# Optimization experiments

Hardware: AMD Instinct MI355X
Metric: run time of the kernel (lower is better)

The kernel has to match this reference:

```python
import jax, jax.numpy as jnp
import numpy as np

B, T, I, H, C = 512, 256, 128, 64, 3  # batch, seq_len, input_size, hidden_size, num_classes


def _lstm_dir(x, w_ih, w_hh, b, reverse):
    """Single-direction LSTM over x: (B, T, D_in) -> (B, T, H).

    Gate order matches PyTorch: i, f, g, o. b = b_ih + b_hh (combined).
    Input-to-gate GEMM is hoisted out of the scan for efficiency.
    """
    xg = jnp.einsum('bti,gi->btg', x, w_ih) + b  # (B, T, 4H)
    if reverse:
        xg = xg[:, ::-1]
    xg_t = jnp.swapaxes(xg, 0, 1)  # (T, B, 4H)
    h0 = jnp.zeros((x.shape[0], w_hh.shape[1]), x.dtype)
    c0 = jnp.zeros_like(h0)

    def step(carry, g):
        h, c = carry
        g = g + h @ w_hh.T
        i, f, gg, o = jnp.split(g, 4, axis=-1)
        i = jax.nn.sigmoid(i)
        f = jax.nn.sigmoid(f)
        gg = jnp.tanh(gg)
        o = jax.nn.sigmoid(o)
        c = f * c + i * gg
        h = o * jnp.tanh(c)
        return (h, c), h

    _, hs = jax.lax.scan(step, (h0, c0), xg_t)  # (T, B, H)
    hs = jnp.swapaxes(hs, 0, 1)  # (B, T, H)
    if reverse:
        hs = hs[:, ::-1]
    return hs


def setup_inputs() -> dict:
    key = jax.random.key(0)
    ks = jax.random.split(key, 20)
    s = 1.0 / np.sqrt(H)  # PyTorch LSTM init scale
    d = {"x": jax.random.normal(ks[0], (B, T, I), dtype=jnp.float32)}
    i = 1
    for l, d_in in [(0, I), (1, 2 * H)]:
        for suf in ["f", "r"]:
            d[f"w_ih_l{l}{suf}"] = jax.random.uniform(ks[i], (4 * H, d_in), minval=-s, maxval=s); i += 1
            d[f"w_hh_l{l}{suf}"] = jax.random.uniform(ks[i], (4 * H, H), minval=-s, maxval=s); i += 1
            d[f"b_l{l}{suf}"] = jax.random.uniform(ks[i], (4 * H,), minval=-s, maxval=s); i += 1
    d["fc_w"] = jax.random.uniform(ks[i], (C, 2 * H), minval=-s, maxval=s); i += 1
    d["fc_b"] = jax.random.uniform(ks[i], (C,), minval=-s, maxval=s)
    return d


def reference(x, w_ih_l0f, w_hh_l0f, b_l0f, w_ih_l0r, w_hh_l0r, b_l0r,
              w_ih_l1f, w_hh_l1f, b_l1f, w_ih_l1r, w_hh_l1r, b_l1r,
              fc_w, fc_b):
    # Layer 0 (bidirectional)
    h0f = _lstm_dir(x, w_ih_l0f, w_hh_l0f, b_l0f, False)
    h0r = _lstm_dir(x, w_ih_l0r, w_hh_l0r, b_l0r, True)
    x1 = jnp.concatenate([h0f, h0r], axis=-1)  # (B, T, 2H)
    # (inter-layer dropout is identity in eval mode)
    # Layer 1 (bidirectional)
    h1f = _lstm_dir(x1, w_ih_l1f, w_hh_l1f, b_l1f, False)
    h1r = _lstm_dir(x1, w_ih_l1r, w_hh_l1r, b_l1r, True)
    out = jnp.concatenate([h1f, h1r], axis=-1)  # (B, T, 2H)
    last = out[:, -1, :]  # (B, 2H); dropout is identity in eval mode
    return last @ fc_w.T + fc_b  # (B, C) logits
```

## Files before the change

kernel.cpp:

```cpp
#include <hip/hip_runtime.h>

#define TT 256
#define BB 512
#define NG 256
#define KIN 128

typedef _Float16 half2v __attribute__((ext_vector_type(2)));
typedef _Float16 half4v __attribute__((ext_vector_type(4)));
typedef _Float16 half8v __attribute__((ext_vector_type(8)));
typedef float float4v __attribute__((ext_vector_type(4)));

__device__ __forceinline__ float sig_(float x){ return 1.f/(1.f+__expf(-x)); }
__device__ __forceinline__ float th_(float x){ return fmaf(2.f, 1.f/(1.f+__expf(-2.f*x)), -1.f); }

#if __has_builtin(__builtin_amdgcn_fdot2)
__device__ __forceinline__ float fdot2_(half2v a, half2v b, float c){
  return __builtin_amdgcn_fdot2(a, b, c, false);
}
#else
__device__ __forceinline__ float fdot2_(half2v a, half2v b, float c){
  return c + (float)a[0]*(float)b[0] + (float)a[1]*(float)b[1];
}
#endif

#define SV2(v,k) __builtin_shufflevector((v),(v), 2*(k), 2*(k)+1)

__device__ __forceinline__ half4v ld4h(const float* p){
  float4v v = *reinterpret_cast<const float4v*>(p);
  half4v h; h[0]=(_Float16)v[0]; h[1]=(_Float16)v[1]; h[2]=(_Float16)v[2]; h[3]=(_Float16)v[3];
  return h;
}

__global__ __launch_bounds__(256)
void conv_weights(const float* __restrict__ s0, const float* __restrict__ s1,
                  const float* __restrict__ s2, const float* __restrict__ s3,
                  const float* __restrict__ s4, const float* __restrict__ s5,
                  _Float16* __restrict__ dst)
{
  const int bid = blockIdx.x, tid = threadIdx.x;
  const float* src; int off, idx;
  if (bid < 128)      { src=s0; off=0;      idx=bid*256+tid; }
  else if (bid < 256) { src=s1; off=32768;  idx=(bid-128)*256+tid; }
  else if (bid < 384) { src=s2; off=65536;  idx=(bid-256)*256+tid; }
  else if (bid < 448) { src=s3; off=98304;  idx=(bid-384)*256+tid; }
  else if (bid < 512) { src=s4; off=114688; idx=(bid-448)*256+tid; }
  else                { src=s5; off=131072; idx=(bid-512)*256+tid; }
  dst[off+idx] = (_Float16)src[idx];
}

template<typename AT>
__global__ __launch_bounds__(256)
void gemm_xg(const AT* __restrict__ A, const _Float16* __restrict__ W16,
             const float* __restrict__ bias, _Float16* __restrict__ Cout)
{
  __shared__ __align__(16) _Float16 aL[64][72];
  __shared__ __align__(16) _Float16 wL[256][72];
  const int tid  = threadIdx.x;
  const int wave = tid >> 6;
  const int lane = tid & 63;
  const int lr   = lane & 15;
  const int kg   = lane >> 4;
  const size_t m0 = (size_t)blockIdx.x * 64;

  float4v acc[4][4];
  #pragma unroll
  for (int a=0;a<4;a++)
    #pragma unroll
    for (int b=0;b<4;b++)
      acc[a][b] = float4v{0.f,0.f,0.f,0.f};

  for (int kc = 0; kc < KIN; kc += 64) {
    if constexpr (__is_same(AT, float)) {
      #pragma unroll
      for (int q=0;q<4;q++){
        int fi = tid + q*256;
        int r = fi >> 4, c4 = (fi & 15)*4;
        *reinterpret_cast<half4v*>(&aL[r][c4]) = ld4h(&A[(m0+(size_t)r)*KIN + kc + c4]);
      }
    } else {
      #pragma unroll
      for (int q=0;q<2;q++){
        int fi = tid + q*256;
        int r = fi >> 3, c8 = (fi & 7)*8;
        *reinterpret_cast<half8v*>(&aL[r][c8]) =
            *reinterpret_cast<const half8v*>(&A[(m0+(size_t)r)*KIN + kc + c8]);
      }
    }
    #pragma unroll
    for (int q=0;q<8;q++){
      int fi = tid + q*256;
      int n = fi >> 3, c8 = (fi & 7)*8;
      *reinterpret_cast<half8v*>(&wL[n][c8]) =
          *reinterpret_cast<const half8v*>(&W16[(size_t)n*KIN + kc + c8]);
    }
    __syncthreads();
    #pragma unroll
    for (int ks=0; ks<64; ks+=32){
      half8v af[4], bf[4];
      #pragma unroll
      for (int rt=0;rt<4;rt++)
        af[rt] = *reinterpret_cast<const half8v*>(&aL[rt*16+lr][ks + kg*8]);
      #pragma unroll
      for (int ct=0;ct<4;ct++)
        bf[ct] = *reinterpret_cast<const half8v*>(&wL[wave*64 + ct*16 + lr][ks + kg*8]);
      #pragma unroll
      for (int rt=0;rt<4;rt++)
        #pragma unroll
        for (int ct=0;ct<4;ct++)
          acc[rt][ct] = __builtin_amdgcn_mfma_f32_16x16x32_f16(af[rt], bf[ct], acc[rt][ct], 0,0,0);
    }
    __syncthreads();
  }
  #pragma unroll
  for (int ct=0;ct<4;ct++){
    const int col = wave*64 + ct*16 + lr;
    const float bv = bias[col];
    #pragma unroll
    for (int rt=0;rt<4;rt++){
      const size_t rbase = m0 + rt*16 + kg*4;
      #pragma unroll
      for (int i=0;i<4;i++)
        Cout[(rbase+(size_t)i)*NG + col] = (_Float16)(acc[rt][ct][i] + bv);
    }
  }
}

template<int MODE>
__global__ __launch_bounds__(256, 4)
void lstm_scan_g4(const _Float16* __restrict__ xgPool,
                  const _Float16* __restrict__ whhPool,
                  int nF,
                  _Float16* __restrict__ x1out, float* __restrict__ hfin)
{
  const int tid = threadIdx.x;
  const int w   = tid >> 6;
  const int j   = tid & 63;
  const bool rev = (int)blockIdx.x >= nF;
  const int b = rev ? ((int)blockIdx.x - nF) : (int)blockIdx.x;
  const _Float16* xg  = xgPool  + (rev ? (size_t)BB*TT*NG : 0);
  const _Float16* whh = whhPool + (rev ? (size_t)16384 : 0);

  __shared__ __align__(16) float acts[2][256];
  __shared__ __align__(16) _Float16 hs4[4][64];

  half8v wreg[8];
  #pragma unroll
  for (int q=0;q<8;q++)
    wreg[q] = *reinterpret_cast<const half8v*>(&whh[(size_t)(w*64 + j)*64 + q*8]);

  hs4[w][j] = (_Float16)0.f;
  float c = 0.f, h_last = 0.f;

  const _Float16* xgb = xg + (size_t)b*TT*NG + w*64 + j;
  _Float16 ring[8];
  #pragma unroll
  for (int u=0;u<8;u++)
    ring[u] = xgb[(size_t)(rev ? (TT-1-u) : u) * NG];

  for (int tb=0; tb<TT; tb+=8){
    #pragma unroll
    for (int u=0;u<8;u++){
      const int tt = tb + u;
      const int t  = rev ? (TT-1-tt) : tt;

      const float xp = (float)ring[u];
      const int tf = tt + 8;
      if (tf < TT)
        ring[u] = xgb[(size_t)(rev ? (TT-1-tf) : tf) * NG];

      float a=0.f, a2=0.f;
      #pragma unroll
      for (int q=0;q<8;q++){
        const half8v h8 = *reinterpret_cast<const half8v*>(&hs4[w][q*8]);
        a  = fdot2_(SV2(wreg[q],0), SV2(h8,0), a);
        a2 = fdot2_(SV2(wreg[q],1), SV2(h8,1), a2);
        a  = fdot2_(SV2(wreg[q],2), SV2(h8,2), a);
        a2 = fdot2_(SV2(wreg[q],3), SV2(h8,3), a2);
      }
      const float pre = xp + (a + a2);
      acts[tt&1][w*64 + j] = (w==2) ? th_(pre) : sig_(pre);
      __syncthreads();

      const float iv = acts[tt&1][j];
      const float fv = acts[tt&1][64+j];
      const float gv = acts[tt&1][128+j];
      const float ov = acts[tt&1][192+j];
      c = fv*c + iv*gv;
      const float h = ov * th_(c);
      h_last = h;
      hs4[w][j] = (_Float16)h;
      if constexpr (MODE==0)
        if (w == 0)
          x1out[((size_t)b*TT + t)*128 + (rev ? 64 : 0) + j] = (_Float16)h;
    }
  }
  if constexpr (MODE==1)
    if (w == 0)
      hfin[(size_t)b*64 + j] = h_last;
}

__global__ __launch_bounds__(256)
void final_fuse(const _Float16* __restrict__ x1, const float* __restrict__ w_ih,
                const float* __restrict__ bvec, const float* __restrict__ hfin,
                const float* __restrict__ fcw, const float* __restrict__ fcb,
                float* __restrict__ out)
{
  const int b = blockIdx.x, tid = threadIdx.x;
  __shared__ float xs[128];
  __shared__ float act[256];
  __shared__ float hall[128];
  if (tid < 128) xs[tid] = (float)x1[((size_t)b*TT + (TT-1))*128 + tid];
  __syncthreads();
  float a = bvec[tid];
  #pragma unroll
  for (int kk=0;kk<32;kk++){
    float4v wv = *reinterpret_cast<const float4v*>(&w_ih[(size_t)tid*128 + kk*4]);
    a += wv[0]*xs[kk*4] + wv[1]*xs[kk*4+1] + wv[2]*xs[kk*4+2] + wv[3]*xs[kk*4+3];
  }
  const int grp = tid>>6;
  act[tid] = (grp==2) ? th_(a) : sig_(a);
  __syncthreads();
  if (tid < 64) {
    float c = act[tid]*act[128+tid];
    float h = act[192+tid]*th_(c);
    hall[64+tid] = h;
    hall[tid] = hfin[(size_t)b*64 + tid];
  }
  __syncthreads();
  if (tid < 3) {
    float acc2 = fcb[tid];
    for (int k=0;k<128;k++) acc2 += fcw[(size_t)tid*128 + k]*hall[k];
    out[(size_t)b*3 + tid] = acc2;
  }
}

extern "C" void kernel_launch(void* const* d_in, const int* in_sizes, int n_in,
                              void* d_out, int out_size, void* d_ws, size_t ws_size,
                              hipStream_t stream) {
  const float* x        = (const float*)d_in[0];
  const float* w_ih_l0f = (const float*)d_in[1];
  const float* w_hh_l0f = (const float*)d_in[2];
  const float* b_l0f    = (const float*)d_in[3];
  const float* w_ih_l0r = (const float*)d_in[4];
  const float* w_hh_l0r = (const float*)d_in[5];
  const float* b_l0r    = (const float*)d_in[6];
  const float* w_ih_l1f = (const float*)d_in[7];
  const float* w_hh_l1f = (const float*)d_in[8];
  const float* b_l1f    = (const float*)d_in[9];
  const float* w_ih_l1r = (const float*)d_in[10];
  const float* b_l1r    = (const float*)d_in[12];
  const float* fc_w     = (const float*)d_in[13];
  const float* fc_b     = (const float*)d_in[14];
  float* out = (float*)d_out;

  const size_t XG_BYTES = (size_t)BB*TT*NG*2;
  const size_t X1_BYTES = (size_t)BB*TT*128*2;
  const size_t HF_BYTES = (size_t)BB*64*4;
  const size_t W16_BYTES = (size_t)147456*2;
  if (ws_size < 2*XG_BYTES + X1_BYTES + HF_BYTES + W16_BYTES) return;
  _Float16* xgF  = (_Float16*)d_ws;
  _Float16* xgR  = (_Float16*)((char*)d_ws + XG_BYTES);
  _Float16* x1   = (_Float16*)((char*)d_ws + 2*XG_BYTES);
  float*    hfin = (float*)   ((char*)d_ws + 2*XG_BYTES + X1_BYTES);
  _Float16* w16  = (_Float16*)((char*)d_ws + 2*XG_BYTES + X1_BYTES + HF_BYTES);
  _Float16* wih_l0f16 = w16;
  _Float16* wih_l0r16 = w16 + 32768;
  _Float16* wih_l1f16 = w16 + 65536;
  _Float16* whh_l0f16 = w16 + 98304;
  _Float16* whh_l1f16 = w16 + 131072;

  const int MBLK = (BB*TT)/64;

  conv_weights<<<576, 256, 0, stream>>>(w_ih_l0f, w_ih_l0r, w_ih_l1f,
                                        w_hh_l0f, w_hh_l0r, w_hh_l1f, w16);
  gemm_xg<float><<<MBLK, 256, 0, stream>>>(x, wih_l0f16, b_l0f, xgF);
  gemm_xg<float><<<MBLK, 256, 0, stream>>>(x, wih_l0r16, b_l0r, xgR);
  lstm_scan_g4<0><<<1024, 256, 0, stream>>>(xgF, whh_l0f16, 512, x1, nullptr);
  gemm_xg<_Float16><<<MBLK, 256, 0, stream>>>(x1, wih_l1f16, b_l1f, xgF);
  lstm_scan_g4<1><<<512, 256, 0, stream>>>(xgF, whh_l1f16, 512, nullptr, hfin);
  final_fuse<<<BB, 256, 0, stream>>>(x1, w_ih_l1r, b_l1r, hfin, fc_w, fc_b, out);
}
```

Before: 402.8 us.

## Batch 16 sequences per block in LSTM scan using MFMA recurrent matmul

Replaces the per-sequence fdot2 recurrence with a block handling 16 batch rows, computing h·W_hh via MFMA 16x16x32 f16 with weights held in registers and h in swizzled LDS. Gate activations are exchanged through LDS in fp16 with two barriers per step. This cuts redundant weight traffic and instruction count per sequence, but launches far fewer blocks (64/32), leaving most CUs idle during the latency-bound serial scan, and stores activations in half precision.

Result: slower. 747.2 us (+85.5%).

```diff
diff --git a/kernel.cpp b/kernel.cpp
--- a/kernel.cpp
+++ b/kernel.cpp
@@ -12,18 +12,6 @@
 
 __device__ __forceinline__ float sig_(float x){ return 1.f/(1.f+__expf(-x)); }
 __device__ __forceinline__ float th_(float x){ return fmaf(2.f, 1.f/(1.f+__expf(-2.f*x)), -1.f); }
-
-#if __has_builtin(__builtin_amdgcn_fdot2)
-__device__ __forceinline__ float fdot2_(half2v a, half2v b, float c){
-  return __builtin_amdgcn_fdot2(a, b, c, false);
-}
-#else
-__device__ __forceinline__ float fdot2_(half2v a, half2v b, float c){
-  return c + (float)a[0]*(float)b[0] + (float)a[1]*(float)b[1];
-}
-#endif
-
-#define SV2(v,k) __builtin_shufflevector((v),(v), 2*(k), 2*(k)+1)
 
 __device__ __forceinline__ half4v ld4h(const float* p){
   float4v v = *reinterpret_cast<const float4v*>(p);
@@ -126,77 +114,131 @@
 }
 
 template<int MODE>
-__global__ __launch_bounds__(256, 4)
-void lstm_scan_g4(const _Float16* __restrict__ xgPool,
+__global__ __launch_bounds__(512, 1)
+void lstm_scan_mf(const _Float16* __restrict__ xgPool,
                   const _Float16* __restrict__ whhPool,
                   int nF,
                   _Float16* __restrict__ x1out, float* __restrict__ hfin)
 {
   const int tid = threadIdx.x;
   const int w   = tid >> 6;
-  const int j   = tid & 63;
+  const int l   = tid & 63;
+  const int g   = w >> 1;
+  const int nh  = w & 1;
+  const int lr  = l & 15;
+  const int kg  = l >> 4;
   const bool rev = (int)blockIdx.x >= nF;
-  const int b = rev ? ((int)blockIdx.x - nF) : (int)blockIdx.x;
+  const int bblk = rev ? ((int)blockIdx.x - nF) : (int)blockIdx.x;
+  const int b0 = bblk * 16;
   const _Float16* xg  = xgPool  + (rev ? (size_t)BB*TT*NG : 0);
   const _Float16* whh = whhPool + (rev ? (size_t)16384 : 0);
 
-  __shared__ __align__(16) float acts[2][256];
-  __shared__ __align__(16) _Float16 hs4[4][64];
-
-  half8v wreg[8];
-  #pragma unroll
-  for (int q=0;q<8;q++)
-    wreg[q] = *reinterpret_cast<const half8v*>(&whh[(size_t)(w*64 + j)*64 + q*8]);
-
-  hs4[w][j] = (_Float16)0.f;
-  float c = 0.f, h_last = 0.f;
-
-  const _Float16* xgb = xg + (size_t)b*TT*NG + w*64 + j;
-  _Float16 ring[8];
-  #pragma unroll
-  for (int u=0;u<8;u++)
-    ring[u] = xgb[(size_t)(rev ? (TT-1-u) : u) * NG];
-
-  for (int tb=0; tb<TT; tb+=8){
-    #pragma unroll
-    for (int u=0;u<8;u++){
-      const int tt = tb + u;
-      const int t  = rev ? (TT-1-tt) : tt;
-
-      const float xp = (float)ring[u];
-      const int tf = tt + 8;
-      if (tf < TT)
-        ring[u] = xgb[(size_t)(rev ? (TT-1-tf) : tf) * NG];
-
-      float a=0.f, a2=0.f;
-      #pragma unroll
-      for (int q=0;q<8;q++){
-        const half8v h8 = *reinterpret_cast<const half8v*>(&hs4[w][q*8]);
-        a  = fdot2_(SV2(wreg[q],0), SV2(h8,0), a);
-        a2 = fdot2_(SV2(wreg[q],1), SV2(h8,1), a2);
-        a  = fdot2_(SV2(wreg[q],2), SV2(h8,2), a);
-        a2 = fdot2_(SV2(wreg[q],3), SV2(h8,3), a2);
-      }
-      const float pre = xp + (a + a2);
-      acts[tt&1][w*64 + j] = (w==2) ? th_(pre) : sig_(pre);
-      __syncthreads();
-
-      const float iv = acts[tt&1][j];
-      const float fv = acts[tt&1][64+j];
-      const float gv = acts[tt&1][128+j];
-      const float ov = acts[tt&1][192+j];
-      c = fv*c + iv*gv;
-      const float h = ov * th_(c);
-      h_last = h;
-      hs4[w][j] = (_Float16)h;
-      if constexpr (MODE==0)
-        if (w == 0)
-          x1out[((size_t)b*TT + t)*128 + (rev ? 64 : 0) + j] = (_Float16)h;
-    }
-  }
-  if constexpr (MODE==1)
-    if (w == 0)
-      hfin[(size_t)b*64 + j] = h_last;
+  __shared__ __align__(16) _Float16 h_lds[16*64];
+  __shared__ __align__(16) _Float16 acts[4*64*20];
+
+  const size_t colA = (size_t)g*64 + (size_t)nh*32 + (size_t)lr;
+  half8v bf00 = *reinterpret_cast<const half8v*>(&whh[(colA   )*64 +  0 + kg*8]);
+  half8v bf01 = *reinterpret_cast<const half8v*>(&whh[(colA   )*64 + 32 + kg*8]);
+  half8v bf10 = *reinterpret_cast<const half8v*>(&whh[(colA+16)*64 +  0 + kg*8]);
+  half8v bf11 = *reinterpret_cast<const half8v*>(&whh[(colA+16)*64 + 32 + kg*8]);
+  asm volatile("" : "+v"(bf00), "+v"(bf01), "+v"(bf10), "+v"(bf11));
+
+  char* hb = (char*)h_lds;
+  const int aswz  = (lr & 7) << 4;
+  const int aoff0 = (lr*128 +  0 + kg*16) ^ aswz;
+  const int aoff1 = (lr*128 + 64 + kg*16) ^ aswz;
+
+  const int awr0 = (g*64 + nh*32 +  0 + lr)*20 + kg*4;
+  const int awr1 = (g*64 + nh*32 + 16 + lr)*20 + kg*4;
+  const int ard0 = (  0 + l)*20 + 2*w;
+  const int ard1 = ( 64 + l)*20 + 2*w;
+  const int ard2 = (128 + l)*20 + 2*w;
+  const int ard3 = (192 + l)*20 + 2*w;
+  const int r0 = 2*w, r1 = 2*w+1;
+  const int hw0 = (r0*128 + l*2) ^ ((r0&7)<<4);
+  const int hw1 = (r1*128 + l*2) ^ ((r1&7)<<4);
+
+  const int t0 = rev ? (TT-1) : 0;
+  const ptrdiff_t dstep = rev ? -(ptrdiff_t)NG : (ptrdiff_t)NG;
+  const _Float16* p0 = xg + ((size_t)(b0 + kg*4 + 0)*TT + t0)*NG + colA;
+  const _Float16* p1 = xg + ((size_t)(b0 + kg*4 + 1)*TT + t0)*NG + colA;
+  const _Float16* p2 = xg + ((size_t)(b0 + kg*4 + 2)*TT + t0)*NG + colA;
+  const _Float16* p3 = xg + ((size_t)(b0 + kg*4 + 3)*TT + t0)*NG + colA;
+
+  half8v sA, sB;
+  sA[0]=p0[0];  sA[1]=p1[0];  sA[2]=p2[0];  sA[3]=p3[0];
+  sA[4]=p0[16]; sA[5]=p1[16]; sA[6]=p2[16]; sA[7]=p3[16];
+  p0+=dstep; p1+=dstep; p2+=dstep; p3+=dstep;
+  sB[0]=p0[0];  sB[1]=p1[0];  sB[2]=p2[0];  sB[3]=p3[0];
+  sB[4]=p0[16]; sB[5]=p1[16]; sB[6]=p2[16]; sB[7]=p3[16];
+  p0+=dstep; p1+=dstep; p2+=dstep; p3+=dstep;
+
+  ((unsigned*)h_lds)[tid] = 0u;
+  float c0 = 0.f, c1 = 0.f, hl0 = 0.f, hl1 = 0.f;
+  __syncthreads();
+
+#define SCAN_STEP(tt_, S_) do {                                              \
+    const int tt = (tt_);                                                    \
+    const int t  = rev ? (TT-1-tt) : tt;                                     \
+    half8v a0 = *reinterpret_cast<const half8v*>(hb + aoff0);                \
+    half8v a1 = *reinterpret_cast<const half8v*>(hb + aoff1);                \
+    float4v ac0, ac1;                                                        \
+    ac0[0]=(float)S_[0]; ac0[1]=(float)S_[1];                                \
+    ac0[2]=(float)S_[2]; ac0[3]=(float)S_[3];                                \
+    ac1[0]=(float)S_[4]; ac1[1]=(float)S_[5];                                \
+    ac1[2]=(float)S_[6]; ac1[3]=(float)S_[7];                                \
+    if (tt+2 < TT){                                                          \
+      S_[0]=p0[0];  S_[1]=p1[0];  S_[2]=p2[0];  S_[3]=p3[0];                 \
+      S_[4]=p0[16]; S_[5]=p1[16]; S_[6]=p2[16]; S_[7]=p3[16];                \
+      p0+=dstep; p1+=dstep; p2+=dstep; p3+=dstep;                            \
+    }                                                                        \
+    ac0 = __builtin_amdgcn_mfma_f32_16x16x32_f16(a0, bf00, ac0, 0,0,0);      \
+    ac0 = __builtin_amdgcn_mfma_f32_16x16x32_f16(a1, bf01, ac0, 0,0,0);      \
+    ac1 = __builtin_amdgcn_mfma_f32_16x16x32_f16(a0, bf10, ac1, 0,0,0);      \
+    ac1 = __builtin_amdgcn_mfma_f32_16x16x32_f16(a1, bf11, ac1, 0,0,0);      \
+    half4v pk0, pk1;                                                         \
+    if (g == 2){                                                             \
+      pk0[0]=(_Float16)th_(ac0[0]); pk0[1]=(_Float16)th_(ac0[1]);            \
+      pk0[2]=(_Float16)th_(ac0[2]); pk0[3]=(_Float16)th_(ac0[3]);            \
+      pk1[0]=(_Float16)th_(ac1[0]); pk1[1]=(_Float16)th_(ac1[1]);            \
+      pk1[2]=(_Float16)th_(ac1[2]); pk1[3]=(_Float16)th_(ac1[3]);            \
+    } else {                                                                 \
+      pk0[0]=(_Float16)sig_(ac0[0]); pk0[1]=(_Float16)sig_(ac0[1]);          \
+      pk0[2]=(_Float16)sig_(ac0[2]); pk0[3]=(_Float16)sig_(ac0[3]);          \
+      pk1[0]=(_Float16)sig_(ac1[0]); pk1[1]=(_Float16)sig_(ac1[1]);          \
+      pk1[2]=(_Float16)sig_(ac1[2]); pk1[3]=(_Float16)sig_(ac1[3]);          \
+    }                                                                        \
+    *reinterpret_cast<half4v*>(&acts[awr0]) = pk0;                           \
+    *reinterpret_cast<half4v*>(&acts[awr1]) = pk1;                           \
+    __syncthreads();                                                         \
+    const half2v vi = *reinterpret_cast<const half2v*>(&acts[ard0]);         \
+    const half2v vf = *reinterpret_cast<const half2v*>(&acts[ard1]);         \
+    const half2v vg = *reinterpret_cast<const half2v*>(&acts[ard2]);         \
+    const half2v vo = *reinterpret_cast<const half2v*>(&acts[ard3]);         \
+    c0 = (float)vf[0]*c0 + (float)vi[0]*(float)vg[0];                        \
+    c1 = (float)vf[1]*c1 + (float)vi[1]*(float)vg[1];                        \
+    const float h0 = (float)vo[0]*th_(c0);                                   \
+    const float h1 = (float)vo[1]*th_(c1);                                   \
+    *reinterpret_cast<_Float16*>(hb + hw0) = (_Float16)h0;                   \
+    *reinterpret_cast<_Float16*>(hb + hw1) = (_Float16)h1;                   \
+    if constexpr (MODE==0){                                                  \
+      const int xoff = rev ? 64 : 0;                                         \
+      x1out[((size_t)(b0+r0)*TT + t)*128 + xoff + l] = (_Float16)h0;         \
+      x1out[((size_t)(b0+r1)*TT + t)*128 + xoff + l] = (_Float16)h1;         \
+    } else { hl0 = h0; hl1 = h1; }                                           \
+    __syncthreads();                                                         \
+  } while(0)
+
+  for (int tb=0; tb<TT; tb+=2){
+    SCAN_STEP(tb,   sA);
+    SCAN_STEP(tb+1, sB);
+  }
+#undef SCAN_STEP
+
+  if constexpr (MODE==1){
+    hfin[(size_t)(b0+r0)*64 + l] = hl0;
+    hfin[(size_t)(b0+r1)*64 + l] = hl1;
+  }
 }
 
 __global__ __launch_bounds__(256)
@@ -275,8 +317,8 @@
                                         w_hh_l0f, w_hh_l0r, w_hh_l1f, w16);
   gemm_xg<float><<<MBLK, 256, 0, stream>>>(x, wih_l0f16, b_l0f, xgF);
   gemm_xg<float><<<MBLK, 256, 0, stream>>>(x, wih_l0r16, b_l0r, xgR);
-  lstm_scan_g4<0><<<1024, 256, 0, stream>>>(xgF, whh_l0f16, 512, x1, nullptr);
+  lstm_scan_mf<0><<<64, 512, 0, stream>>>(xgF, whh_l0f16, 32, x1, nullptr);
   gemm_xg<_Float16><<<MBLK, 256, 0, stream>>>(x1, wih_l1f16, b_l1f, xgF);
-  lstm_scan_g4<1><<<512, 256, 0, stream>>>(xgF, whh_l1f16, 512, nullptr, hfin);
+  lstm_scan_mf<1><<<32, 512, 0, stream>>>(xgF, whh_l1f16, 32, nullptr, hfin);
   final_fuse<<<BB, 256, 0, stream>>>(x1, w_ih_l1r, b_l1r, hfin, fc_w, fc_b, out);
 }
```

## Batch four sequences per LSTM scan block with LDS-resident transposed weights

Applied to the files above, without the earlier changes.

The recurrent scan now processes four batch rows per block. W_hh is stored transposed and interleaved in LDS and shared across those rows, and each thread computes one gate column for all four rows with packed fp16 FMA instead of fp32-accumulated fdot2. This cuts the block count fourfold and amortises weight and h reads across batch rows. In exchange it adds a second barrier per step, lowers occupancy (launch bounds 1, only 256/128 blocks for 256 CUs), and accumulates in fp16, which risks precision loss.

Measured after the change: 697.3 us. 1.73x slower.

```diff
diff --git a/kernel.cpp b/kernel.cpp
--- a/kernel.cpp
+++ b/kernel.cpp
@@ -13,17 +13,17 @@
 __device__ __forceinline__ float sig_(float x){ return 1.f/(1.f+__expf(-x)); }
 __device__ __forceinline__ float th_(float x){ return fmaf(2.f, 1.f/(1.f+__expf(-2.f*x)), -1.f); }
 
-#if __has_builtin(__builtin_amdgcn_fdot2)
-__device__ __forceinline__ float fdot2_(half2v a, half2v b, float c){
-  return __builtin_amdgcn_fdot2(a, b, c, false);
+#define SV2(v,k) __builtin_shufflevector((v),(v), 2*(k), 2*(k)+1)
+
+#if __has_builtin(__builtin_elementwise_fma)
+__device__ __forceinline__ half2v pkfma_(half2v a, half2v b, half2v c){
+  return __builtin_elementwise_fma(a, b, c);
 }
 #else
-__device__ __forceinline__ float fdot2_(half2v a, half2v b, float c){
-  return c + (float)a[0]*(float)b[0] + (float)a[1]*(float)b[1];
+__device__ __forceinline__ half2v pkfma_(half2v a, half2v b, half2v c){
+  return a*b + c;
 }
 #endif
-
-#define SV2(v,k) __builtin_shufflevector((v),(v), 2*(k), 2*(k)+1)
 
 __device__ __forceinline__ half4v ld4h(const float* p){
   float4v v = *reinterpret_cast<const float4v*>(p);
@@ -38,14 +38,20 @@
                   _Float16* __restrict__ dst)
 {
   const int bid = blockIdx.x, tid = threadIdx.x;
-  const float* src; int off, idx;
+  const float* src; int off, idx; bool tr = false;
   if (bid < 128)      { src=s0; off=0;      idx=bid*256+tid; }
   else if (bid < 256) { src=s1; off=32768;  idx=(bid-128)*256+tid; }
   else if (bid < 384) { src=s2; off=65536;  idx=(bid-256)*256+tid; }
-  else if (bid < 448) { src=s3; off=98304;  idx=(bid-384)*256+tid; }
-  else if (bid < 512) { src=s4; off=114688; idx=(bid-448)*256+tid; }
-  else                { src=s5; off=131072; idx=(bid-512)*256+tid; }
-  dst[off+idx] = (_Float16)src[idx];
+  else if (bid < 448) { src=s3; off=98304;  idx=(bid-384)*256+tid; tr=true; }
+  else if (bid < 512) { src=s4; off=114688; idx=(bid-448)*256+tid; tr=true; }
+  else                { src=s5; off=131072; idx=(bid-512)*256+tid; tr=true; }
+  if (!tr){
+    dst[off+idx] = (_Float16)src[idx];
+  } else {
+    const int col = idx >> 6, k = idx & 63;
+    const int kk = k >> 3, e = k & 7;
+    dst[off + (kk*256 + col)*8 + e] = (_Float16)src[idx];
+  }
 }
 
 template<typename AT>
@@ -126,77 +132,114 @@
 }
 
 template<int MODE>
-__global__ __launch_bounds__(256, 4)
-void lstm_scan_g4(const _Float16* __restrict__ xgPool,
-                  const _Float16* __restrict__ whhPool,
-                  int nF,
-                  _Float16* __restrict__ x1out, float* __restrict__ hfin)
+__global__ __launch_bounds__(256, 1)
+void lstm_scan_lds(const _Float16* __restrict__ xgPool,
+                   const _Float16* __restrict__ whhTP,
+                   int nF,
+                   _Float16* __restrict__ x1out, float* __restrict__ hfin)
 {
-  const int tid = threadIdx.x;
-  const int w   = tid >> 6;
-  const int j   = tid & 63;
+  const int l = threadIdx.x;
+  const int w = l >> 6;
+  const int j = l & 63;
   const bool rev = (int)blockIdx.x >= nF;
-  const int b = rev ? ((int)blockIdx.x - nF) : (int)blockIdx.x;
-  const _Float16* xg  = xgPool  + (rev ? (size_t)BB*TT*NG : 0);
-  const _Float16* whh = whhPool + (rev ? (size_t)16384 : 0);
-
-  __shared__ __align__(16) float acts[2][256];
-  __shared__ __align__(16) _Float16 hs4[4][64];
-
-  half8v wreg[8];
+  const int bblk = rev ? ((int)blockIdx.x - nF) : (int)blockIdx.x;
+  const int b0 = bblk * 4;
+  const _Float16* xg   = xgPool + (rev ? (size_t)BB*TT*NG : 0);
+  const _Float16* whhT = whhTP  + (rev ? (size_t)16384 : 0);
+
+  __shared__ __align__(16) _Float16 wlds[16384];
+  __shared__ __align__(16) float    acts[4][256];
+  __shared__ __align__(16) _Float16 hlds[4][64];
+
   #pragma unroll
-  for (int q=0;q<8;q++)
-    wreg[q] = *reinterpret_cast<const half8v*>(&whh[(size_t)(w*64 + j)*64 + q*8]);
-
-  hs4[w][j] = (_Float16)0.f;
+  for (int q=0;q<8;q++){
+    const int u = q*256 + l;
+    *reinterpret_cast<half8v*>(&wlds[u*8]) =
+        *reinterpret_cast<const half8v*>(&whhT[(size_t)u*8]);
+  }
+  if (l < 128) ((unsigned*)hlds)[l] = 0u;
   float c = 0.f, h_last = 0.f;
-
-  const _Float16* xgb = xg + (size_t)b*TT*NG + w*64 + j;
-  _Float16 ring[8];
-  #pragma unroll
-  for (int u=0;u<8;u++)
-    ring[u] = xgb[(size_t)(rev ? (TT-1-u) : u) * NG];
-
-  for (int tb=0; tb<TT; tb+=8){
-    #pragma unroll
-    for (int u=0;u<8;u++){
-      const int tt = tb + u;
-      const int t  = rev ? (TT-1-tt) : tt;
-
-      const float xp = (float)ring[u];
-      const int tf = tt + 8;
-      if (tf < TT)
-        ring[u] = xgb[(size_t)(rev ? (TT-1-tf) : tf) * NG];
-
-      float a=0.f, a2=0.f;
-      #pragma unroll
-      for (int q=0;q<8;q++){
-        const half8v h8 = *reinterpret_cast<const half8v*>(&hs4[w][q*8]);
-        a  = fdot2_(SV2(wreg[q],0), SV2(h8,0), a);
-        a2 = fdot2_(SV2(wreg[q],1), SV2(h8,1), a2);
-        a  = fdot2_(SV2(wreg[q],2), SV2(h8,2), a);
-        a2 = fdot2_(SV2(wreg[q],3), SV2(h8,3), a2);
-      }
-      const float pre = xp + (a + a2);
-      acts[tt&1][w*64 + j] = (w==2) ? th_(pre) : sig_(pre);
-      __syncthreads();
-
-      const float iv = acts[tt&1][j];
-      const float fv = acts[tt&1][64+j];
-      const float gv = acts[tt&1][128+j];
-      const float ov = acts[tt&1][192+j];
-      c = fv*c + iv*gv;
-      const float h = ov * th_(c);
-      h_last = h;
-      hs4[w][j] = (_Float16)h;
-      if constexpr (MODE==0)
-        if (w == 0)
-          x1out[((size_t)b*TT + t)*128 + (rev ? 64 : 0) + j] = (_Float16)h;
-    }
-  }
+  __syncthreads();
+
+  const int t0 = rev ? (TT-1) : 0;
+  const ptrdiff_t dstep = rev ? -(ptrdiff_t)NG : (ptrdiff_t)NG;
+  const _Float16* p0 = xg + ((size_t)(b0+0)*TT + t0)*NG + l;
+  const _Float16* p1 = xg + ((size_t)(b0+1)*TT + t0)*NG + l;
+  const _Float16* p2 = xg + ((size_t)(b0+2)*TT + t0)*NG + l;
+  const _Float16* p3 = xg + ((size_t)(b0+3)*TT + t0)*NG + l;
+
+  half4v sA, sB;
+  sA[0]=*p0; sA[1]=*p1; sA[2]=*p2; sA[3]=*p3;
+  p0+=dstep; p1+=dstep; p2+=dstep; p3+=dstep;
+  sB[0]=*p0; sB[1]=*p1; sB[2]=*p2; sB[3]=*p3;
+  p0+=dstep; p1+=dstep; p2+=dstep; p3+=dstep;
+
+#define SCAN_STEP(tt_, S_) do {                                               \
+    const int tt = (tt_);                                                     \
+    const int t  = rev ? (TT-1-tt) : tt;                                      \
+    const float xr0=(float)S_[0], xr1=(float)S_[1];                           \
+    const float xr2=(float)S_[2], xr3=(float)S_[3];                           \
+    if (tt+2 < TT){                                                           \
+      S_[0]=*p0; S_[1]=*p1; S_[2]=*p2; S_[3]=*p3;                             \
+      p0+=dstep; p1+=dstep; p2+=dstep; p3+=dstep;                             \
+    }                                                                         \
+    half2v a00={0,0},a01={0,0},a02={0,0},a03={0,0};                           \
+    half2v a10={0,0},a11={0,0},a12={0,0},a13={0,0};                           \
+    half2v a20={0,0},a21={0,0},a22={0,0},a23={0,0};                           \
+    half2v a30={0,0},a31={0,0},a32={0,0},a33={0,0};                           \
+    _Pragma("unroll")                                                         \
+    for (int kk=0;kk<8;kk++){                                                 \
+      const half8v w8 = *reinterpret_cast<const half8v*>(&wlds[(kk*256+l)*8]);\
+      const half8v h0 = *reinterpret_cast<const half8v*>(&hlds[0][kk*8]);     \
+      const half8v h1 = *reinterpret_cast<const half8v*>(&hlds[1][kk*8]);     \
+      const half8v h2 = *reinterpret_cast<const half8v*>(&hlds[2][kk*8]);     \
+      const half8v h3 = *reinterpret_cast<const half8v*>(&hlds[3][kk*8]);     \
+      a00=pkfma_(SV2(w8,0),SV2(h0,0),a00); a01=pkfma_(SV2(w8,1),SV2(h0,1),a01);\
+      a02=pkfma_(SV2(w8,2),SV2(h0,2),a02); a03=pkfma_(SV2(w8,3),SV2(h0,3),a03);\
+      a10=pkfma_(SV2(w8,0),SV2(h1,0),a10); a11=pkfma_(SV2(w8,1),SV2(h1,1),a11);\
+      a12=pkfma_(SV2(w8,2),SV2(h1,2),a12); a13=pkfma_(SV2(w8,3),SV2(h1,3),a13);\
+      a20=pkfma_(SV2(w8,0),SV2(h2,0),a20); a21=pkfma_(SV2(w8,1),SV2(h2,1),a21);\
+      a22=pkfma_(SV2(w8,2),SV2(h2,2),a22); a23=pkfma_(SV2(w8,3),SV2(h2,3),a23);\
+      a30=pkfma_(SV2(w8,0),SV2(h3,0),a30); a31=pkfma_(SV2(w8,1),SV2(h3,1),a31);\
+      a32=pkfma_(SV2(w8,2),SV2(h3,2),a32); a33=pkfma_(SV2(w8,3),SV2(h3,3),a33);\
+    }                                                                         \
+    const half2v s0 = (a00+a01)+(a02+a03);                                    \
+    const half2v s1 = (a10+a11)+(a12+a13);                                    \
+    const half2v s2 = (a20+a21)+(a22+a23);                                    \
+    const half2v s3 = (a30+a31)+(a32+a33);                                    \
+    const float pre0 = xr0 + (float)s0[0] + (float)s0[1];                     \
+    const float pre1 = xr1 + (float)s1[0] + (float)s1[1];                     \
+    const float pre2 = xr2 + (float)s2[0] + (float)s2[1];                     \
+    const float pre3 = xr3 + (float)s3[0] + (float)s3[1];                     \
+    if (w == 2){                                                              \
+      acts[0][l]=th_(pre0); acts[1][l]=th_(pre1);                             \
+      acts[2][l]=th_(pre2); acts[3][l]=th_(pre3);                             \
+    } else {                                                                  \
+      acts[0][l]=sig_(pre0); acts[1][l]=sig_(pre1);                           \
+      acts[2][l]=sig_(pre2); acts[3][l]=sig_(pre3);                           \
+    }                                                                         \
+    __syncthreads();                                                          \
+    const float iv = acts[w][j];                                              \
+    const float fv = acts[w][64+j];                                           \
+    const float gv = acts[w][128+j];                                          \
+    const float ov = acts[w][192+j];                                          \
+    c = fv*c + iv*gv;                                                         \
+    const float h = ov * th_(c);                                              \
+    h_last = h;                                                               \
+    hlds[w][j] = (_Float16)h;                                                 \
+    if constexpr (MODE==0)                                                    \
+      x1out[((size_t)(b0+w)*TT + t)*128 + (rev ? 64 : 0) + j] = (_Float16)h;  \
+    __syncthreads();                                                          \
+  } while(0)
+
+  for (int tb=0; tb<TT; tb+=2){
+    SCAN_STEP(tb,   sA);
+    SCAN_STEP(tb+1, sB);
+  }
+#undef SCAN_STEP
+
   if constexpr (MODE==1)
-    if (w == 0)
-      hfin[(size_t)b*64 + j] = h_last;
+    hfin[(size_t)(b0+w)*64 + j] = h_last;
 }
 
 __global__ __launch_bounds__(256)
@@ -266,8 +309,8 @@
   _Float16* wih_l0f16 = w16;
   _Float16* wih_l0r16 = w16 + 32768;
   _Float16* wih_l1f16 = w16 + 65536;
-  _Float16* whh_l0f16 = w16 + 98304;
-  _Float16* whh_l1f16 = w16 + 131072;
+  _Float16* whhT_l0f  = w16 + 98304;
+  _Float16* whhT_l1f  = w16 + 131072;
 
   const int MBLK = (BB*TT)/64;
 
@@ -275,8 +318,8 @@
                                         w_hh_l0f, w_hh_l0r, w_hh_l1f, w16);
   gemm_xg<float><<<MBLK, 256, 0, stream>>>(x, wih_l0f16, b_l0f, xgF);
   gemm_xg<float><<<MBLK, 256, 0, stream>>>(x, wih_l0r16, b_l0r, xgR);
-  lstm_scan_g4<0><<<1024, 256, 0, stream>>>(xgF, whh_l0f16, 512, x1, nullptr);
+  lstm_scan_lds<0><<<256, 256, 0, stream>>>(xgF, whhT_l0f, 128, x1, nullptr);
   gemm_xg<_Float16><<<MBLK, 256, 0, stream>>>(x1, wih_l1f16, b_l1f, xgF);
-  lstm_scan_g4<1><<<512, 256, 0, stream>>>(xgF, whh_l1f16, 512, nullptr, hfin);
+  lstm_scan_lds<1><<<128, 256, 0, stream>>>(xgF, whhT_l1f, 128, nullptr, hfin);
   final_fuse<<<BB, 256, 0, stream>>>(x1, w_ih_l1r, b_l1r, hfin, fc_w, fc_b, out);
 }
```

## Batch 16 sequences per block and use MFMA for recurrent LSTM matmul

Applied to the files above, without the earlier changes.

Replaces the per-sequence scan kernel, which used fdot2 with one batch row per block, with a kernel that handles 16 batch rows per block. The recurrent h@W_hh product runs on 16x16x32 f16 MFMA instructions, with W_hh staged in swizzled LDS and h double-buffered in LDS. Each lane now owns four gate columns across four batch rows, which removes the acts exchange and one barrier per step. The cost is a much smaller grid (64 and 32 blocks instead of 1024 and 512), so far fewer CUs are busy, and each serial step carries MFMA latency plus LDS reads of the full weight matrix.

Result: slower. 624.4 us (+55.0%).

```diff
diff --git a/kernel.cpp b/kernel.cpp
--- a/kernel.cpp
+++ b/kernel.cpp
@@ -12,18 +12,6 @@
 
 __device__ __forceinline__ float sig_(float x){ return 1.f/(1.f+__expf(-x)); }
 __device__ __forceinline__ float th_(float x){ return fmaf(2.f, 1.f/(1.f+__expf(-2.f*x)), -1.f); }
-
-#if __has_builtin(__builtin_amdgcn_fdot2)
-__device__ __forceinline__ float fdot2_(half2v a, half2v b, float c){
-  return __builtin_amdgcn_fdot2(a, b, c, false);
-}
-#else
-__device__ __forceinline__ float fdot2_(half2v a, half2v b, float c){
-  return c + (float)a[0]*(float)b[0] + (float)a[1]*(float)b[1];
-}
-#endif
-
-#define SV2(v,k) __builtin_shufflevector((v),(v), 2*(k), 2*(k)+1)
 
 __device__ __forceinline__ half4v ld4h(const float* p){
   float4v v = *reinterpret_cast<const float4v*>(p);
@@ -126,77 +114,159 @@
 }
 
 template<int MODE>
-__global__ __launch_bounds__(256, 4)
-void lstm_scan_g4(const _Float16* __restrict__ xgPool,
+__global__ __launch_bounds__(256, 1)
+void lstm_scan_mm(const _Float16* __restrict__ xgPool,
                   const _Float16* __restrict__ whhPool,
                   int nF,
                   _Float16* __restrict__ x1out, float* __restrict__ hfin)
 {
   const int tid = threadIdx.x;
   const int w   = tid >> 6;
-  const int j   = tid & 63;
+  const int l   = tid & 63;
+  const int lr  = l & 15;
+  const int kg  = l >> 4;
   const bool rev = (int)blockIdx.x >= nF;
-  const int b = rev ? ((int)blockIdx.x - nF) : (int)blockIdx.x;
+  const int bblk = rev ? ((int)blockIdx.x - nF) : (int)blockIdx.x;
+  const int b0 = bblk * 16;
   const _Float16* xg  = xgPool  + (rev ? (size_t)BB*TT*NG : 0);
   const _Float16* whh = whhPool + (rev ? (size_t)16384 : 0);
 
-  __shared__ __align__(16) float acts[2][256];
-  __shared__ __align__(16) _Float16 hs4[4][64];
-
-  half8v wreg[8];
-  #pragma unroll
-  for (int q=0;q<8;q++)
-    wreg[q] = *reinterpret_cast<const half8v*>(&whh[(size_t)(w*64 + j)*64 + q*8]);
-
-  hs4[w][j] = (_Float16)0.f;
-  float c = 0.f, h_last = 0.f;
-
-  const _Float16* xgb = xg + (size_t)b*TT*NG + w*64 + j;
-  _Float16 ring[8];
-  #pragma unroll
-  for (int u=0;u<8;u++)
-    ring[u] = xgb[(size_t)(rev ? (TT-1-u) : u) * NG];
-
-  for (int tb=0; tb<TT; tb+=8){
-    #pragma unroll
-    for (int u=0;u<8;u++){
-      const int tt = tb + u;
-      const int t  = rev ? (TT-1-tt) : tt;
-
-      const float xp = (float)ring[u];
-      const int tf = tt + 8;
-      if (tf < TT)
-        ring[u] = xgb[(size_t)(rev ? (TT-1-tf) : tf) * NG];
-
-      float a=0.f, a2=0.f;
-      #pragma unroll
-      for (int q=0;q<8;q++){
-        const half8v h8 = *reinterpret_cast<const half8v*>(&hs4[w][q*8]);
-        a  = fdot2_(SV2(wreg[q],0), SV2(h8,0), a);
-        a2 = fdot2_(SV2(wreg[q],1), SV2(h8,1), a2);
-        a  = fdot2_(SV2(wreg[q],2), SV2(h8,2), a);
-        a2 = fdot2_(SV2(wreg[q],3), SV2(h8,3), a2);
-      }
-      const float pre = xp + (a + a2);
-      acts[tt&1][w*64 + j] = (w==2) ? th_(pre) : sig_(pre);
-      __syncthreads();
-
-      const float iv = acts[tt&1][j];
-      const float fv = acts[tt&1][64+j];
-      const float gv = acts[tt&1][128+j];
-      const float ov = acts[tt&1][192+j];
-      c = fv*c + iv*gv;
-      const float h = ov * th_(c);
-      h_last = h;
-      hs4[w][j] = (_Float16)h;
-      if constexpr (MODE==0)
-        if (w == 0)
-          x1out[((size_t)b*TT + t)*128 + (rev ? 64 : 0) + j] = (_Float16)h;
-    }
-  }
-  if constexpr (MODE==1)
-    if (w == 0)
-      hfin[(size_t)b*64 + j] = h_last;
+  __shared__ __align__(16) _Float16 wlds[16384];
+  __shared__ __align__(16) _Float16 hlds[2][1024];
+
+  #pragma unroll
+  for (int q=0;q<8;q++){
+    const int u = q*256 + tid;
+    const int col = u >> 3, k8 = u & 7;
+    const int byte = (col*128 + k8*16) ^ ((col & 7) << 4);
+    *reinterpret_cast<half8v*>((char*)wlds + byte) =
+        *reinterpret_cast<const half8v*>(&whh[(size_t)u*8]);
+  }
+  ((unsigned*)hlds)[tid]     = 0u;
+  ((unsigned*)hlds)[tid+256] = 0u;
+  float cc0=0.f, cc1=0.f, cc2=0.f, cc3=0.f;
+  float hl0=0.f, hl1=0.f, hl2=0.f, hl3=0.f;
+  __syncthreads();
+
+  const int swz  = (lr & 7) << 4;
+  const int aof0 = (lr*128 +  0 + kg*16) ^ swz;
+  const int aof1 = (lr*128 + 64 + kg*16) ^ swz;
+  const int cA   = w*16 + lr;
+  int bof[4][2];
+  #pragma unroll
+  for (int g=0; g<4; ++g){
+    const int col = g*64 + cA;
+    bof[g][0] = (col*128 +  0 + kg*16) ^ ((col & 7) << 4);
+    bof[g][1] = (col*128 + 64 + kg*16) ^ ((col & 7) << 4);
+  }
+  int hw[4];
+  #pragma unroll
+  for (int i=0;i<4;i++){
+    const int r = kg*4 + i;
+    hw[i] = (r*128 + cA*2) ^ ((r & 7) << 4);
+  }
+  char* hb = (char*)hlds;
+  char* wb = (char*)wlds;
+
+  const int t0i = rev ? (TT-1) : 0;
+  const ptrdiff_t dstep = rev ? -(ptrdiff_t)NG : (ptrdiff_t)NG;
+  const _Float16* p0 = xg + ((size_t)(b0+kg*4+0)*TT + t0i)*NG + cA;
+  const _Float16* p1 = xg + ((size_t)(b0+kg*4+1)*TT + t0i)*NG + cA;
+  const _Float16* p2 = xg + ((size_t)(b0+kg*4+2)*TT + t0i)*NG + cA;
+  const _Float16* p3 = xg + ((size_t)(b0+kg*4+3)*TT + t0i)*NG + cA;
+
+  _Float16 rgA[16], rgB[16];
+#define REFILL(S_) do {                                            \
+    S_[0]=p0[0];    S_[1]=p1[0];    S_[2]=p2[0];    S_[3]=p3[0];   \
+    S_[4]=p0[64];   S_[5]=p1[64];   S_[6]=p2[64];   S_[7]=p3[64];  \
+    S_[8]=p0[128];  S_[9]=p1[128];  S_[10]=p2[128]; S_[11]=p3[128];\
+    S_[12]=p0[192]; S_[13]=p1[192]; S_[14]=p2[192]; S_[15]=p3[192];\
+    p0+=dstep; p1+=dstep; p2+=dstep; p3+=dstep;                    \
+  } while(0)
+  REFILL(rgA);
+  REFILL(rgB);
+
+  const int xoff = rev ? 64 : 0;
+  _Float16* q0 = x1out ? x1out + ((size_t)(b0+kg*4+0)*TT)*128 + xoff + cA : nullptr;
+  _Float16* q1 = x1out ? x1out + ((size_t)(b0+kg*4+1)*TT)*128 + xoff + cA : nullptr;
+  _Float16* q2 = x1out ? x1out + ((size_t)(b0+kg*4+2)*TT)*128 + xoff + cA : nullptr;
+  _Float16* q3 = x1out ? x1out + ((size_t)(b0+kg*4+3)*TT)*128 + xoff + cA : nullptr;
+
+#define SCAN_STEP(tt_, S_) do {                                              \
+    const int tt = (tt_);                                                    \
+    const int t  = rev ? (TT-1-tt) : tt;                                     \
+    const int p  = tt & 1;                                                   \
+                                  \
+    float4v ac0, ac1, ac2, ac3;                                              \
+    ac0[0]=(float)S_[0];  ac0[1]=(float)S_[1];                               \
+    ac0[2]=(float)S_[2];  ac0[3]=(float)S_[3];                               \
+    ac1[0]=(float)S_[4];  ac1[1]=(float)S_[5];                               \
+    ac1[2]=(float)S_[6];  ac1[3]=(float)S_[7];                               \
+    ac2[0]=(float)S_[8];  ac2[1]=(float)S_[9];                               \
+    ac2[2]=(float)S_[10]; ac2[3]=(float)S_[11];                              \
+    ac3[0]=(float)S_[12]; ac3[1]=(float)S_[13];                              \
+    ac3[2]=(float)S_[14]; ac3[3]=(float)S_[15];                              \
+    if (tt+2 < TT) REFILL(S_);                                               \
+                                                  \
+    const half8v a0 = *reinterpret_cast<const half8v*>(hb + p*2048 + aof0);  \
+    const half8v a1 = *reinterpret_cast<const half8v*>(hb + p*2048 + aof1);  \
+                                              \
+    const half8v b00 = *reinterpret_cast<const half8v*>(wb + bof[0][0]);     \
+    const half8v b01 = *reinterpret_cast<const half8v*>(wb + bof[0][1]);     \
+    const half8v b10 = *reinterpret_cast<const half8v*>(wb + bof[1][0]);     \
+    const half8v b11 = *reinterpret_cast<const half8v*>(wb + bof[1][1]);     \
+    const half8v b20 = *reinterpret_cast<const half8v*>(wb + bof[2][0]);     \
+    const half8v b21 = *reinterpret_cast<const half8v*>(wb + bof[2][1]);     \
+    const half8v b30 = *reinterpret_cast<const half8v*>(wb + bof[3][0]);     \
+    const half8v b31 = *reinterpret_cast<const half8v*>(wb + bof[3][1]);     \
+    ac0 = __builtin_amdgcn_mfma_f32_16x16x32_f16(a0, b00, ac0, 0,0,0);       \
+    ac1 = __builtin_amdgcn_mfma_f32_16x16x32_f16(a0, b10, ac1, 0,0,0);       \
+    ac2 = __builtin_amdgcn_mfma_f32_16x16x32_f16(a0, b20, ac2, 0,0,0);       \
+    ac3 = __builtin_amdgcn_mfma_f32_16x16x32_f16(a0, b30, ac3, 0,0,0);       \
+    ac0 = __builtin_amdgcn_mfma_f32_16x16x32_f16(a1, b01, ac0, 0,0,0);       \
+    ac1 = __builtin_amdgcn_mfma_f32_16x16x32_f16(a1, b11, ac1, 0,0,0);       \
+    ac2 = __builtin_amdgcn_mfma_f32_16x16x32_f16(a1, b21, ac2, 0,0,0);       \
+    ac3 = __builtin_amdgcn_mfma_f32_16x16x32_f16(a1, b31, ac3, 0,0,0);       \
+                                  \
+    {                                                                        \
+      const float i0=sig_(ac0[0]), f0=sig_(ac1[0]), g0=th_(ac2[0]), o0=sig_(ac3[0]); \
+      const float i1=sig_(ac0[1]), f1=sig_(ac1[1]), g1=th_(ac2[1]), o1=sig_(ac3[1]); \
+      const float i2=sig_(ac0[2]), f2=sig_(ac1[2]), g2=th_(ac2[2]), o2=sig_(ac3[2]); \
+      const float i3=sig_(ac0[3]), f3=sig_(ac1[3]), g3=th_(ac2[3]), o3=sig_(ac3[3]); \
+      cc0 = f0*cc0 + i0*g0;  cc1 = f1*cc1 + i1*g1;                           \
+      cc2 = f2*cc2 + i2*g2;  cc3 = f3*cc3 + i3*g3;                           \
+      const float h0v = o0*th_(cc0), h1v = o1*th_(cc1);                      \
+      const float h2v = o2*th_(cc2), h3v = o3*th_(cc3);                      \
+      char* hp = hb + (p^1)*2048;                                            \
+      *reinterpret_cast<_Float16*>(hp + hw[0]) = (_Float16)h0v;              \
+      *reinterpret_cast<_Float16*>(hp + hw[1]) = (_Float16)h1v;              \
+      *reinterpret_cast<_Float16*>(hp + hw[2]) = (_Float16)h2v;              \
+      *reinterpret_cast<_Float16*>(hp + hw[3]) = (_Float16)h3v;              \
+      if constexpr (MODE==0){                                                \
+        q0[(size_t)t*128] = (_Float16)h0v;                                   \
+        q1[(size_t)t*128] = (_Float16)h1v;                                   \
+        q2[(size_t)t*128] = (_Float16)h2v;                                   \
+        q3[(size_t)t*128] = (_Float16)h3v;                                   \
+      } else {                                                               \
+        hl0=h0v; hl1=h1v; hl2=h2v; hl3=h3v;                                  \
+      }                                                                      \
+    }                                                                        \
+    __syncthreads();                                                         \
+  } while(0)
+
+  for (int tb=0; tb<TT; tb+=2){
+    SCAN_STEP(tb,   rgA);
+    SCAN_STEP(tb+1, rgB);
+  }
+#undef SCAN_STEP
+#undef REFILL
+
+  if constexpr (MODE==1){
+    hfin[(size_t)(b0+kg*4+0)*64 + cA] = hl0;
+    hfin[(size_t)(b0+kg*4+1)*64 + cA] = hl1;
+    hfin[(size_t)(b0+kg*4+2)*64 + cA] = hl2;
+    hfin[(size_t)(b0+kg*4+3)*64 + cA] = hl3;
+  }
 }
 
 __global__ __launch_bounds__(256)
@@ -275,8 +345,8 @@
                                         w_hh_l0f, w_hh_l0r, w_hh_l1f, w16);
   gemm_xg<float><<<MBLK, 256, 0, stream>>>(x, wih_l0f16, b_l0f, xgF);
   gemm_xg<float><<<MBLK, 256, 0, stream>>>(x, wih_l0r16, b_l0r, xgR);
-  lstm_scan_g4<0><<<1024, 256, 0, stream>>>(xgF, whh_l0f16, 512, x1, nullptr);
+  lstm_scan_mm<0><<<64, 256, 0, stream>>>(xgF, whh_l0f16, 32, x1, nullptr);
   gemm_xg<_Float16><<<MBLK, 256, 0, stream>>>(x1, wih_l1f16, b_l1f, xgF);
-  lstm_scan_g4<1><<<512, 256, 0, stream>>>(xgF, whh_l1f16, 512, nullptr, hfin);
+  lstm_scan_mm<1><<<32, 256, 0, stream>>>(xgF, whh_l1f16, 32, nullptr, hfin);
   final_fuse<<<BB, 256, 0, stream>>>(x1, w_ih_l1r, b_l1r, hfin, fc_w, fc_b, out);
 }
```
